# Performance work log

Hardware: AMD Instinct MI355X
Metric: run time of the kernel (lower is better)

## Reference

```python
import jax, jax.numpy as jnp
import numpy as np

OUT, IN, GROUP, RANK, NPROT, BATCH = 4096, 4096, 128, 32, 32, 4096


def setup_inputs() -> dict:
    key = jax.random.key(0)
    k = jax.random.split(key, 7)
    n = OUT * IN
    x = jax.random.normal(k[0], (BATCH, IN), dtype=jnp.float32)
    # two int4 values per byte; byte values in [0,256)
    packed_int4 = jax.random.randint(k[1], (n // 2,), 0, 256, dtype=jnp.int32)
    # positive per-group scales (typical int4 scale magnitudes)
    scales = jax.random.uniform(k[2], (IN // GROUP,), dtype=jnp.float32, minval=0.005, maxval=0.02)
    svd_u = jax.random.normal(k[3], (OUT, RANK), dtype=jnp.float32) * 0.01
    svd_v = jax.random.normal(k[4], (IN, RANK), dtype=jnp.float32) * 0.01
    protected_channels = jax.random.normal(k[5], (NPROT, IN), dtype=jnp.float32) * 0.02
    # unique protected row indices
    protected_indices = jax.random.permutation(k[6], OUT)[:NPROT].astype(jnp.int32)
    return {
        "x": x,
        "packed_int4": packed_int4,
        "scales": scales,
        "svd_u": svd_u,
        "svd_v": svd_v,
        "protected_channels": protected_channels,
        "protected_indices": protected_indices,
    }


def reference(x, packed_int4, scales, svd_u, svd_v, protected_channels, protected_indices):
    out_f = svd_u.shape[0]
    in_f = x.shape[-1]
    group = in_f // scales.shape[0]
    # Unpack: original puts low nibbles in first half of the flat array,
    # high nibbles in the second half (split layout, not interleaved).
    lo = packed_int4 & 15
    hi = (packed_int4 >> 4) & 15
    unpacked = jnp.concatenate([lo, hi])  # [out*in]
    w_quant = (unpacked.astype(jnp.float32) - 8.0).reshape(out_f, in_f)
    # per-group dequant over input columns
    w = (w_quant.reshape(out_f, -1, group) * scales[None, :, None]).reshape(out_f, in_f)
    # low-rank SVD correction
    w = w + svd_u @ svd_v.T
    # protected output channels overwrite full rows
    w = w.at[protected_indices].set(protected_channels)
    out = x @ w.T  # [batch, out]
    return out.astype(jnp.float16)
```

## Files before the change

kernel.cpp:

```cpp
#include <hip/hip_runtime.h>
#include <hip/hip_bf16.h>
#include <hip/hip_fp16.h>

#define OUT_F 4096
#define IN_F  4096
#define BATCH 4096
#define RANK  32
#define KPAD  4160
#define NKB   130
#define NT    65

typedef __hip_bfloat16 bf16;
using bf16x8 = __attribute__((ext_vector_type(8))) short;
using f32x4  = __attribute__((ext_vector_type(4))) float;


__device__ __forceinline__ void gload_lds16(const void* g, void* l) {
  __builtin_amdgcn_global_load_lds(
      (const __attribute__((address_space(1))) unsigned int*)g,
      (__attribute__((address_space(3))) unsigned int*)l,
      16, 0, 0);
}

__device__ __forceinline__ unsigned short bf16_bits(float f) {
  bf16 h = __float2bfloat16(f);
  return *(unsigned short*)&h;
}

#define SBAR() asm volatile("s_barrier" ::: "memory")

__global__ __launch_bounds__(256) void prep_xs(const float* __restrict__ x,
                                               const float* __restrict__ scales,
                                               bf16* __restrict__ A) {
  int bid  = blockIdx.x;
  int rb   = bid >> 1;
  int half = bid & 1;
  int t = threadIdx.x;
  int lane = t & 63;
  int row = lane & 15, koct = lane >> 4;
  const float* xr = x + (size_t)(rb * 16 + row) * IN_F;
  for (int k32 = (t >> 6) + half * 4; k32 < NKB; k32 += 8) {
    int k = k32 * 32 + koct * 8;
    bf16x8 pk = (bf16x8){0, 0, 0, 0, 0, 0, 0, 0};
    if (k < IN_F) {
      float sv = scales[k >> 7];
      float4 v0 = *(const float4*)(xr + k);
      float4 v1 = *(const float4*)(xr + k + 4);
      pk[0] = (short)bf16_bits(v0.x * sv);
      pk[1] = (short)bf16_bits(v0.y * sv);
      pk[2] = (short)bf16_bits(v0.z * sv);
      pk[3] = (short)bf16_bits(v0.w * sv);
      pk[4] = (short)bf16_bits(v1.x * sv);
      pk[5] = (short)bf16_bits(v1.y * sv);
      pk[6] = (short)bf16_bits(v1.z * sv);
      pk[7] = (short)bf16_bits(v1.w * sv);
    }
    *(bf16x8*)(A + ((size_t)rb * NKB + k32) * 512 + (size_t)lane * 8) = pk;
  }
}

__global__ __launch_bounds__(256) void prep_misc(const float* __restrict__ v,
                                                 const float* __restrict__ scales,
                                                 const float* __restrict__ u,
                                                 bf16* __restrict__ vst,
                                                 bf16* __restrict__ B) {
  int bid = blockIdx.x;
  if (bid < 512) {
    int gid = bid * 256 + threadIdx.x;
    int c = gid >> 5, r = gid & 31;
    float val = v[(size_t)c * RANK + r] / scales[c >> 7];
    vst[(size_t)r * IN_F + c] = __float2bfloat16(val);
  } else {
    int i = (bid - 512) * 256 + threadIdx.x;
    int o = i >> 6, j = i & 63;
    float val = (j < RANK) ? u[o * RANK + j] : 0.f;
    B[(size_t)o * KPAD + IN_F + j] = __float2bfloat16(val);
  }
}

__global__ __launch_bounds__(64) void prep_t_mfma(const bf16* __restrict__ Af,
                                                  const bf16* __restrict__ vst,
                                                  bf16* __restrict__ Aw) {
  int lane = threadIdx.x;
  int rb = blockIdx.x;
  const bf16* abase = Af + (size_t)rb * NKB * 512 + (size_t)lane * 8;
  const bf16* brow0 = vst + (size_t)(lane & 15) * IN_F + ((lane >> 4) << 3);
  const bf16* brow1 = vst + (size_t)(16 + (lane & 15)) * IN_F + ((lane >> 4) << 3);
  f32x4 acc0 = (f32x4){0.f, 0.f, 0.f, 0.f};
  f32x4 acc1 = (f32x4){0.f, 0.f, 0.f, 0.f};
#pragma unroll 8
  for (int k32 = 0; k32 < 128; ++k32) {
    bf16x8 av  = *(const bf16x8*)(abase + (size_t)k32 * 512);
    bf16x8 bv0 = *(const bf16x8*)(brow0 + k32 * 32);
    bf16x8 bv1 = *(const bf16x8*)(brow1 + k32 * 32);
    acc0 = __builtin_amdgcn_mfma_f32_16x16x32_bf16(av, bv0, acc0, 0, 0, 0);
    acc1 = __builtin_amdgcn_mfma_f32_16x16x32_bf16(av, bv1, acc1, 0, 0, 0);
  }
  bf16* base = Aw + ((size_t)rb * NKB + 128) * 512;
  int c0 = lane & 15, c1 = 16 + (lane & 15);
#pragma unroll
  for (int r = 0; r < 4; ++r) {
    int row15 = ((lane >> 4) << 2) + r;
    base[(c0 >> 3) * 128 + row15 * 8 + (c0 & 7)] = __float2bfloat16(acc0[r]);
    base[(c1 >> 3) * 128 + row15 * 8 + (c1 & 7)] = __float2bfloat16(acc1[r]);
  }
}

__global__ __launch_bounds__(256) void prep_b(const int* __restrict__ packed,
                                              bf16* __restrict__ B) {
  size_t i = (size_t)blockIdx.x * 256 + threadIdx.x;
  int4 p = ((const int4*)packed)[i];
  size_t e = i * 4;
  int o = (int)(e >> 12);
  int c = (int)(e & 4095);
  int vals[4] = {p.x, p.y, p.z, p.w};
  unsigned short lo[4], hi[4];
#pragma unroll
  for (int j = 0; j < 4; ++j) {
    lo[j] = bf16_bits((float)((vals[j] & 15) - 8));
    hi[j] = bf16_bits((float)(((vals[j] >> 4) & 15) - 8));
  }
  *(ushort4*)(B + (size_t)o * KPAD + c) = make_ushort4(lo[0], lo[1], lo[2], lo[3]);
  *(ushort4*)(B + (size_t)(o + 2048) * KPAD + c) = make_ushort4(hi[0], hi[1], hi[2], hi[3]);
}

__global__ __launch_bounds__(256) void prep_prot(const float* __restrict__ pc,
                                                 const float* __restrict__ scales,
                                                 const int* __restrict__ pidx,
                                                 bf16* __restrict__ B) {
  int bi = blockIdx.x;
  int row = pidx[bi];
  bf16* Br = B + (size_t)row * KPAD;
  for (int c = threadIdx.x; c < KPAD; c += 256) {
    float val = (c < IN_F) ? pc[(size_t)bi * IN_F + c] / scales[c >> 7] : 0.f;
    Br[c] = __float2bfloat16(val);
  }
}

__global__ __launch_bounds__(512, 2) void gemm_bt(const bf16* __restrict__ A,
                                                  const bf16* __restrict__ B,
                                                  float* __restrict__ out) {
  __shared__ __align__(16) bf16 Bs[4 * 256 * 64];

  int bid = blockIdx.x;
  int swz = (bid & 7) * 32 + (bid >> 3);
  int brow = (swz >> 4) << 8;
  int bcol = (swz & 15) << 8;

  int tid = threadIdx.x;
  int lane = tid & 63;
  int wave = tid >> 6;
  int wr = wave >> 1;
  int wc = wave & 1;

  f32x4 acc[4][8];
#pragma unroll
  for (int m = 0; m < 4; ++m)
#pragma unroll
    for (int n = 0; n < 8; ++n)
      acc[m][n] = (f32x4){0.f, 0.f, 0.f, 0.f};

  const char* abase[4];
  int rbw = (brow >> 4) + wr * 4;
#pragma unroll
  for (int m = 0; m < 4; ++m)
    abase[m] = (const char*)A + ((size_t)(rbw + m) * NKB) * 1024 + lane * 16;

  int boff[8];
#pragma unroll
  for (int n = 0; n < 8; ++n) {
    int rbr = wc * 128 + n * 16 + (lane & 15);
    int s0 = (lane >> 4) ^ (rbr & 7);
    boff[n] = rbr * 128 + (s0 << 4);
  }

  const bf16* gB[4]; int lB[4];
#pragma unroll
  for (int q = 0; q < 4; ++q) {
    int idx = q * 512 + tid;
    int row = idx >> 3, slot = idx & 7;
    gB[q] = B + (size_t)(bcol + row) * KPAD + ((slot ^ (row & 7)) << 3);
    lB[q] = idx << 4;
  }
  char* bs0 = (char*)Bs;

  bf16x8 a0[4][2], a1[4][2];
#pragma unroll
  for (int m = 0; m < 4; ++m)
#pragma unroll
    for (int kk = 0; kk < 2; ++kk)
      a0[m][kk] = *(const bf16x8*)(abase[m] + kk * 1024);
#pragma unroll
  for (int kt = 0; kt < 3; ++kt)
#pragma unroll
    for (int q = 0; q < 4; ++q)
      gload_lds16(gB[q] + kt * 64, bs0 + kt * 32768 + lB[q]);
  asm volatile("s_waitcnt vmcnt(8)" ::: "memory");
  SBAR();

  auto tile_body = [&](int t, bf16x8 (&Au)[4][2], bf16x8 (&Ap)[4][2], bool pref) {
    const char* rb_ = bs0 + (t & 3) * 32768;
    char* wb = bs0 + ((t + 3) & 3) * 32768;
    int kt = (t + 3 < NT) ? (t + 3) : (NT - 1);
#pragma unroll
    for (int p = 0; p < 4; ++p) {
      if (p == 0 && pref) {
#pragma unroll
        for (int m = 0; m < 4; ++m)
#pragma unroll
          for (int kk = 0; kk < 2; ++kk)
            Ap[m][kk] = *(const bf16x8*)(abase[m] + (size_t)(2 * (t + 1) + kk) * 1024);
      }
      bf16x8 bv0k0 = *(const bf16x8*)(rb_ + boff[2 * p]);
      bf16x8 bv0k1 = *(const bf16x8*)(rb_ + (boff[2 * p] ^ 64));
      bf16x8 bv1k0 = *(const bf16x8*)(rb_ + boff[2 * p + 1]);
      bf16x8 bv1k1 = *(const bf16x8*)(rb_ + (boff[2 * p + 1] ^ 64));
      gload_lds16(gB[p] + (size_t)kt * 64, wb + lB[p]);
      __builtin_amdgcn_s_setprio(1);
#pragma unroll
      for (int m = 0; m < 4; ++m) {
        acc[m][2 * p]     = __builtin_amdgcn_mfma_f32_16x16x32_bf16(Au[m][0], bv0k0, acc[m][2 * p], 0, 0, 0);
        acc[m][2 * p]     = __builtin_amdgcn_mfma_f32_16x16x32_bf16(Au[m][1], bv0k1, acc[m][2 * p], 0, 0, 0);
        acc[m][2 * p + 1] = __builtin_amdgcn_mfma_f32_16x16x32_bf16(Au[m][0], bv1k0, acc[m][2 * p + 1], 0, 0, 0);
        acc[m][2 * p + 1] = __builtin_amdgcn_mfma_f32_16x16x32_bf16(Au[m][1], bv1k1, acc[m][2 * p + 1], 0, 0, 0);
      }
      __builtin_amdgcn_s_setprio(0);
    }
    asm volatile("s_waitcnt vmcnt(4)" ::: "memory");
    SBAR();
  };

  for (int t = 0; t < NT - 1; t += 2) {
    tile_body(t, a0, a1, true);
    tile_body(t + 1, a1, a0, true);
  }
  tile_body(NT - 1, a0, a1, false);

#pragma unroll
  for (int m = 0; m < 4; ++m)
#pragma unroll
    for (int n = 0; n < 8; ++n)
#pragma unroll
      for (int r = 0; r < 4; ++r) {
        int mm = brow + wr * 64 + m * 16 + ((lane >> 4) << 2) + r;
        int nn = bcol + wc * 128 + n * 16 + (lane & 15);
        out[(size_t)mm * OUT_F + nn] = __half2float(__float2half(acc[m][n][r]));
      }
  asm volatile("s_waitcnt vmcnt(0)" ::: "memory");
}

extern "C" void kernel_launch(void* const* d_in, const int* in_sizes, int n_in,
                              void* d_out, int out_size, void* d_ws, size_t ws_size,
                              hipStream_t stream) {
  const float* x      = (const float*)d_in[0];
  const int*   packed = (const int*)d_in[1];
  const float* scales = (const float*)d_in[2];
  const float* svd_u  = (const float*)d_in[3];
  const float* svd_v  = (const float*)d_in[4];
  const float* pc     = (const float*)d_in[5];
  const int*   pidx   = (const int*)d_in[6];
  float* out = (float*)d_out;

  bf16* A   = (bf16*)d_ws;
  bf16* B   = A + (size_t)BATCH * KPAD;
  bf16* vst = B + (size_t)OUT_F * KPAD;

  prep_xs    <<<512,   256, 0, stream>>>(x, scales, A);
  prep_misc  <<<1536,  256, 0, stream>>>(svd_v, scales, svd_u, vst, B);
  prep_t_mfma<<<256,   64,  0, stream>>>(A, vst, A);
  prep_b     <<<8192,  256, 0, stream>>>(packed, B);
  prep_prot  <<<32,    256, 0, stream>>>(pc, scales, pidx, B);
  gemm_bt    <<<256,   512, 0, stream>>>(A, B, out);
}
```

Measured before the change: 328.5 us.

## Fuse preprocessing kernels: merge x-scaling with low-rank projection, fold protected rows

Merges the x-scaling/packing kernel with the x·V low-rank projection into one 512-thread kernel. It transposes x tiles through swizzled LDS, splits the K reduction across 8 waves and reduces the partials in LDS. Protected-row handling moves into the weight unpack kernel, and the U columns of protected rows are zeroed in prep_misc. This cuts kernel launches and replaces a 64-thread-per-block serial MFMA pass with a wider one. In exchange, every unpack thread scans the 32 protected indices and the padding block is written explicitly.

```diff
diff --git a/kernel.cpp b/kernel.cpp
--- a/kernel.cpp
+++ b/kernel.cpp
@@ -29,39 +29,10 @@
 
 #define SBAR() asm volatile("s_barrier" ::: "memory")
 
-__global__ __launch_bounds__(256) void prep_xs(const float* __restrict__ x,
-                                               const float* __restrict__ scales,
-                                               bf16* __restrict__ A) {
-  int bid  = blockIdx.x;
-  int rb   = bid >> 1;
-  int half = bid & 1;
-  int t = threadIdx.x;
-  int lane = t & 63;
-  int row = lane & 15, koct = lane >> 4;
-  const float* xr = x + (size_t)(rb * 16 + row) * IN_F;
-  for (int k32 = (t >> 6) + half * 4; k32 < NKB; k32 += 8) {
-    int k = k32 * 32 + koct * 8;
-    bf16x8 pk = (bf16x8){0, 0, 0, 0, 0, 0, 0, 0};
-    if (k < IN_F) {
-      float sv = scales[k >> 7];
-      float4 v0 = *(const float4*)(xr + k);
-      float4 v1 = *(const float4*)(xr + k + 4);
-      pk[0] = (short)bf16_bits(v0.x * sv);
-      pk[1] = (short)bf16_bits(v0.y * sv);
-      pk[2] = (short)bf16_bits(v0.z * sv);
-      pk[3] = (short)bf16_bits(v0.w * sv);
-      pk[4] = (short)bf16_bits(v1.x * sv);
-      pk[5] = (short)bf16_bits(v1.y * sv);
-      pk[6] = (short)bf16_bits(v1.z * sv);
-      pk[7] = (short)bf16_bits(v1.w * sv);
-    }
-    *(bf16x8*)(A + ((size_t)rb * NKB + k32) * 512 + (size_t)lane * 8) = pk;
-  }
-}
-
 __global__ __launch_bounds__(256) void prep_misc(const float* __restrict__ v,
                                                  const float* __restrict__ scales,
                                                  const float* __restrict__ u,
+                                                 const int* __restrict__ pidx,
                                                  bf16* __restrict__ vst,
                                                  bf16* __restrict__ B) {
   int bid = blockIdx.x;
@@ -74,45 +45,103 @@
     int i = (bid - 512) * 256 + threadIdx.x;
     int o = i >> 6, j = i & 63;
     float val = (j < RANK) ? u[o * RANK + j] : 0.f;
+#pragma unroll
+    for (int jj = 0; jj < 32; ++jj)
+      if (pidx[jj] == o) val = 0.f;
     B[(size_t)o * KPAD + IN_F + j] = __float2bfloat16(val);
   }
 }
 
-__global__ __launch_bounds__(64) void prep_t_mfma(const bf16* __restrict__ Af,
-                                                  const bf16* __restrict__ vst,
-                                                  bf16* __restrict__ Aw) {
-  int lane = threadIdx.x;
+__global__ __launch_bounds__(512) void prep_a(const float* __restrict__ x,
+                                              const float* __restrict__ scales,
+                                              const bf16* __restrict__ vst,
+                                              bf16* __restrict__ A) {
+  __shared__ __align__(16) char lds[16384];
   int rb = blockIdx.x;
-  const bf16* abase = Af + (size_t)rb * NKB * 512 + (size_t)lane * 8;
-  const bf16* brow0 = vst + (size_t)(lane & 15) * IN_F + ((lane >> 4) << 3);
-  const bf16* brow1 = vst + (size_t)(16 + (lane & 15)) * IN_F + ((lane >> 4) << 3);
+  int tid = threadIdx.x, w = tid >> 6, l = tid & 63;
+
+  for (int c = 0; c < 8; ++c) {
+#pragma unroll
+    for (int j = 0; j < 2; ++j) {
+      int r = w * 2 + j;
+      const float* xr = x + (size_t)(rb * 16 + r) * IN_F + c * 512 + l * 8;
+      float sv = scales[(c * 512 + l * 8) >> 7];
+      float4 v0 = *(const float4*)xr;
+      float4 v1 = *(const float4*)(xr + 4);
+      bf16x8 pk;
+      pk[0] = (short)bf16_bits(v0.x * sv); pk[1] = (short)bf16_bits(v0.y * sv);
+      pk[2] = (short)bf16_bits(v0.z * sv); pk[3] = (short)bf16_bits(v0.w * sv);
+      pk[4] = (short)bf16_bits(v1.x * sv); pk[5] = (short)bf16_bits(v1.y * sv);
+      pk[6] = (short)bf16_bits(v1.z * sv); pk[7] = (short)bf16_bits(v1.w * sv);
+      int kb = l >> 2;
+      int byte = kb * 1024 + (((l & 3) << 4) + r) * 16;
+      *(bf16x8*)(lds + (byte ^ ((kb & 7) << 4))) = pk;
+    }
+    __syncthreads();
+#pragma unroll
+    for (int j = 0; j < 2; ++j) {
+      int f = w * 2 + j;
+      int byte = f * 1024 + l * 16;
+      bf16x8 pk = *(const bf16x8*)(lds + (byte ^ ((f & 7) << 4)));
+      *(bf16x8*)(A + ((size_t)rb * NKB + c * 16 + f) * 512 + (size_t)l * 8) = pk;
+    }
+    __syncthreads();
+  }
+
+  const bf16* abase = A + (size_t)rb * NKB * 512 + (size_t)l * 8;
+  const bf16* brow0 = vst + (size_t)(l & 15) * IN_F + ((l >> 4) << 3);
+  const bf16* brow1 = vst + (size_t)(16 + (l & 15)) * IN_F + ((l >> 4) << 3);
   f32x4 acc0 = (f32x4){0.f, 0.f, 0.f, 0.f};
   f32x4 acc1 = (f32x4){0.f, 0.f, 0.f, 0.f};
 #pragma unroll 8
-  for (int k32 = 0; k32 < 128; ++k32) {
+  for (int k32 = w * 16; k32 < w * 16 + 16; ++k32) {
     bf16x8 av  = *(const bf16x8*)(abase + (size_t)k32 * 512);
     bf16x8 bv0 = *(const bf16x8*)(brow0 + k32 * 32);
     bf16x8 bv1 = *(const bf16x8*)(brow1 + k32 * 32);
     acc0 = __builtin_amdgcn_mfma_f32_16x16x32_bf16(av, bv0, acc0, 0, 0, 0);
     acc1 = __builtin_amdgcn_mfma_f32_16x16x32_bf16(av, bv1, acc1, 0, 0, 0);
   }
-  bf16* base = Aw + ((size_t)rb * NKB + 128) * 512;
-  int c0 = lane & 15, c1 = 16 + (lane & 15);
-#pragma unroll
-  for (int r = 0; r < 4; ++r) {
-    int row15 = ((lane >> 4) << 2) + r;
-    base[(c0 >> 3) * 128 + row15 * 8 + (c0 & 7)] = __float2bfloat16(acc0[r]);
-    base[(c1 >> 3) * 128 + row15 * 8 + (c1 & 7)] = __float2bfloat16(acc1[r]);
+  *(f32x4*)(lds + w * 2048 + l * 32)      = acc0;
+  *(f32x4*)(lds + w * 2048 + l * 32 + 16) = acc1;
+  __syncthreads();
+  if (w == 1) {
+    bf16x8 z = (bf16x8){0, 0, 0, 0, 0, 0, 0, 0};
+    *(bf16x8*)(A + ((size_t)rb * NKB + 129) * 512 + (size_t)l * 8) = z;
+  }
+  if (w == 0) {
+#pragma unroll
+    for (int ww = 1; ww < 8; ++ww) {
+      acc0 += *(const f32x4*)(lds + ww * 2048 + l * 32);
+      acc1 += *(const f32x4*)(lds + ww * 2048 + l * 32 + 16);
+    }
+    bf16* base = A + ((size_t)rb * NKB + 128) * 512;
+    int c0 = l & 15, c1 = 16 + (l & 15);
+#pragma unroll
+    for (int r = 0; r < 4; ++r) {
+      int row15 = ((l >> 4) << 2) + r;
+      base[(c0 >> 3) * 128 + row15 * 8 + (c0 & 7)] = __float2bfloat16(acc0[r]);
+      base[(c1 >> 3) * 128 + row15 * 8 + (c1 & 7)] = __float2bfloat16(acc1[r]);
+    }
   }
 }
 
 __global__ __launch_bounds__(256) void prep_b(const int* __restrict__ packed,
+                                              const float* __restrict__ pc,
+                                              const float* __restrict__ scales,
+                                              const int* __restrict__ pidx,
                                               bf16* __restrict__ B) {
   size_t i = (size_t)blockIdx.x * 256 + threadIdx.x;
   int4 p = ((const int4*)packed)[i];
   size_t e = i * 4;
   int o = (int)(e >> 12);
   int c = (int)(e & 4095);
+  int pi_lo = -1, pi_hi = -1;
+#pragma unroll
+  for (int j = 0; j < 32; ++j) {
+    int pr = pidx[j];
+    if (pr == o) pi_lo = j;
+    if (pr == o + 2048) pi_hi = j;
+  }
   int vals[4] = {p.x, p.y, p.z, p.w};
   unsigned short lo[4], hi[4];
 #pragma unroll
@@ -120,21 +149,20 @@
     lo[j] = bf16_bits((float)((vals[j] & 15) - 8));
     hi[j] = bf16_bits((float)(((vals[j] >> 4) & 15) - 8));
   }
+  if (pi_lo >= 0) {
+    float sv = scales[c >> 7];
+#pragma unroll
+    for (int j = 0; j < 4; ++j)
+      lo[j] = bf16_bits(pc[(size_t)pi_lo * IN_F + c + j] / sv);
+  }
+  if (pi_hi >= 0) {
+    float sv = scales[c >> 7];
+#pragma unroll
+    for (int j = 0; j < 4; ++j)
+      hi[j] = bf16_bits(pc[(size_t)pi_hi * IN_F + c + j] / sv);
+  }
   *(ushort4*)(B + (size_t)o * KPAD + c) = make_ushort4(lo[0], lo[1], lo[2], lo[3]);
   *(ushort4*)(B + (size_t)(o + 2048) * KPAD + c) = make_ushort4(hi[0], hi[1], hi[2], hi[3]);
-}
-
-__global__ __launch_bounds__(256) void prep_prot(const float* __restrict__ pc,
-                                                 const float* __restrict__ scales,
-                                                 const int* __restrict__ pidx,
-                                                 bf16* __restrict__ B) {
-  int bi = blockIdx.x;
-  int row = pidx[bi];
-  bf16* Br = B + (size_t)row * KPAD;
-  for (int c = threadIdx.x; c < KPAD; c += 256) {
-    float val = (c < IN_F) ? pc[(size_t)bi * IN_F + c] / scales[c >> 7] : 0.f;
-    Br[c] = __float2bfloat16(val);
-  }
 }
 
 __global__ __launch_bounds__(512, 2) void gemm_bt(const bf16* __restrict__ A,
@@ -265,10 +293,8 @@
   bf16* B   = A + (size_t)BATCH * KPAD;
   bf16* vst = B + (size_t)OUT_F * KPAD;
 
-  prep_xs    <<<512,   256, 0, stream>>>(x, scales, A);
-  prep_misc  <<<1536,  256, 0, stream>>>(svd_v, scales, svd_u, vst, B);
-  prep_t_mfma<<<256,   64,  0, stream>>>(A, vst, A);
-  prep_b     <<<8192,  256, 0, stream>>>(packed, B);
-  prep_prot  <<<32,    256, 0, stream>>>(pc, scales, pidx, B);
-  gemm_bt    <<<256,   512, 0, stream>>>(A, B, out);
-}
+  prep_misc<<<1536, 256, 0, stream>>>(svd_v, scales, svd_u, pidx, vst, B);
+  prep_a   <<<256,  512, 0, stream>>>(x, scales, vst, A);
+  prep_b   <<<8192, 256, 0, stream>>>(packed, pc, scales, pidx, B);
+  gemm_bt  <<<256,  512, 0, stream>>>(A, B, out);
+}
```

New measurement: 289.5 us. 11.9% less time.
